# Optimization experiments

Measured on AMD Instinct MI355X. Metric: run time of the kernel, lower is better.

The kernel has to match this reference:

```python
import jax, jax.numpy as jnp
import numpy as np

ENC, PRED, H, V, DMAX = 1024, 640, 640, 1024, 4
B, T, U = 4, 256, 64


def setup_inputs() -> dict:
    key = jax.random.key(0)
    ks = jax.random.split(key, 10)
    s = lambda d: 1.0 / np.sqrt(d)
    return {
        "encoder_out": jax.random.normal(ks[0], (B, T, ENC), jnp.float32),
        "predictor_out": jax.random.normal(ks[1], (B, U, PRED), jnp.float32),
        "W_enc": jax.random.uniform(ks[2], (H, ENC), jnp.float32, -s(ENC), s(ENC)),
        "b_enc": jax.random.uniform(ks[3], (H,), jnp.float32, -s(ENC), s(ENC)),
        "W_pred": jax.random.uniform(ks[4], (H, PRED), jnp.float32, -s(PRED), s(PRED)),
        "b_pred": jax.random.uniform(ks[5], (H,), jnp.float32, -s(PRED), s(PRED)),
        "W_out": jax.random.uniform(ks[6], (V, H), jnp.float32, -s(H), s(H)),
        "b_out": jax.random.uniform(ks[7], (V,), jnp.float32, -s(H), s(H)),
        "W_dur": jax.random.uniform(ks[8], (DMAX + 1, H), jnp.float32, -s(H), s(H)),
        "b_dur": jax.random.uniform(ks[9], (DMAX + 1,), jnp.float32, -s(H), s(H)),
    }


def reference(encoder_out, predictor_out, W_enc, b_enc, W_pred, b_pred,
              W_out, b_out, W_dur, b_dur):
    # Project encoder [B,T,H] and predictor [B,U,H]
    enc = jnp.einsum('bte,he->bth', encoder_out, W_enc) + b_enc
    pred = jnp.einsum('bup,hp->buh', predictor_out, W_pred) + b_pred
    # Broadcast-add -> [B,T,U,H], tanh
    joint = jnp.tanh(enc[:, :, None, :] + pred[:, None, :, :])
    # Dual heads
    logits = jnp.einsum('btuh,vh->btuv', joint, W_out) + b_out        # [B,T,U,V]
    durations = jnp.einsum('btuh,dh->btud', joint, W_dur) + b_dur     # [B,T,U,DMAX+1]
    return (logits, durations)
```

## Files before the change

kernel.cpp:

```cpp
#include <hip/hip_runtime.h>

typedef unsigned short u16;
typedef unsigned int u32;

typedef __bf16 bf16x8 __attribute__((ext_vector_type(8)));
typedef float f32x4 __attribute__((ext_vector_type(4)));

union FragI { int4 i; bf16x8 b; };
union FragU { bf16x8 b; u16 u[8]; };

__device__ __forceinline__ u16 f2bf(float x) {
  u32 u = __float_as_uint(x);
  u32 r = (u + 0x7fffu + ((u >> 16) & 1u)) >> 16;
  return (u16)r;
}

__device__ __forceinline__ float tanh_fast(float x) {
  float e = __expf(2.0f * x);
  return 1.0f - __fdividef(2.0f, e + 1.0f);
}

__device__ __forceinline__ bf16x8 load_cvt8(const float* __restrict__ p) {
  float4 f0 = *(const float4*)p;
  float4 f1 = *(const float4*)(p + 4);
  FragU t;
  t.u[0] = f2bf(f0.x); t.u[1] = f2bf(f0.y); t.u[2] = f2bf(f0.z); t.u[3] = f2bf(f0.w);
  t.u[4] = f2bf(f1.x); t.u[5] = f2bf(f1.y); t.u[6] = f2bf(f1.z); t.u[7] = f2bf(f1.w);
  return t.b;
}

#define GLDS(gptr, lptr) \
  __builtin_amdgcn_global_load_lds((const __attribute__((address_space(1))) u32*)(gptr), \
                                   (__attribute__((address_space(3))) u32*)(lptr), 16, 0, 0)

__global__ __launch_bounds__(256) void conv_v4(const float* __restrict__ in,
                                               u16* __restrict__ out, int n4) {
  int i = blockIdx.x * 256 + threadIdx.x;
  if (i >= n4) return;
  float4 f = ((const float4*)in)[i];
  union { u16 u[4]; int2 v; } o;
  o.u[0] = f2bf(f.x); o.u[1] = f2bf(f.y); o.u[2] = f2bf(f.z); o.u[3] = f2bf(f.w);
  ((int2*)out)[i] = o.v;
}

__global__ __launch_bounds__(256) void proj_gemm(const float* __restrict__ A,
                                                 const float* __restrict__ Bw,
                                                 const float* __restrict__ bias,
                                                 float* __restrict__ C,
                                                 int M, int N, int K) {
  int tid = threadIdx.x;
  int lane = tid & 63, wid = tid >> 6;
  int m0 = blockIdx.x * 64, n0 = blockIdx.y * 64;
  int kper = K >> 2;
  int kbase = wid * kper;
  int ksteps = kper >> 5;
  int r16 = lane & 15, khi = (lane >> 4) * 8;

  f32x4 z = {0.f, 0.f, 0.f, 0.f};
  f32x4 acc[4][4];
  for (int i = 0; i < 4; ++i)
    for (int j = 0; j < 4; ++j) acc[i][j] = z;

  for (int ks = 0; ks < ksteps; ++ks) {
    int k = kbase + ks * 32 + khi;
    bf16x8 af[4], bf[4];
#pragma unroll
    for (int fm = 0; fm < 4; ++fm)
      af[fm] = load_cvt8(A + (size_t)(m0 + fm * 16 + r16) * K + k);
#pragma unroll
    for (int fn = 0; fn < 4; ++fn)
      bf[fn] = load_cvt8(Bw + (size_t)(n0 + fn * 16 + r16) * K + k);
#pragma unroll
    for (int fm = 0; fm < 4; ++fm)
#pragma unroll
      for (int fn = 0; fn < 4; ++fn)
        acc[fm][fn] = __builtin_amdgcn_mfma_f32_16x16x32_bf16(af[fm], bf[fn], acc[fm][fn], 0, 0, 0);
  }

  __shared__ float red[4][64][64];
#pragma unroll
  for (int fm = 0; fm < 4; ++fm)
#pragma unroll
    for (int fn = 0; fn < 4; ++fn)
#pragma unroll
      for (int i = 0; i < 4; ++i)
        red[wid][fm * 16 + (lane >> 4) * 4 + i][fn * 16 + r16] = acc[fm][fn][i];
  __syncthreads();
  for (int idx = tid; idx < 4096; idx += 256) {
    int r = idx >> 6, c = idx & 63;
    float s = red[0][r][c] + red[1][r][c] + red[2][r][c] + red[3][r][c] + bias[n0 + c];
    C[(size_t)(m0 + r) * N + n0 + c] = s;
  }
}

__global__ __launch_bounds__(256) void joint_tanh(const float* __restrict__ enc,
                                                  const float* __restrict__ pred,
                                                  u16* __restrict__ J) {
  const int total = 65536 * 80;
  for (int c = blockIdx.x * 256 + threadIdx.x; c < total; c += gridDim.x * 256) {
    int m = c / 80;
    int j = c - m * 80;
    int bt = m >> 6;
    int uu = m & 63;
    int b = bt >> 8;
    const float* ep = enc + bt * 640 + j * 8;
    const float* pp = pred + (b * 64 + uu) * 640 + j * 8;
    float4 e0 = *(const float4*)ep;
    float4 e1 = *(const float4*)(ep + 4);
    float4 p0 = *(const float4*)pp;
    float4 p1 = *(const float4*)(pp + 4);
    union { u16 u[8]; int4 v; } o;
    o.u[0] = f2bf(tanh_fast(e0.x + p0.x));
    o.u[1] = f2bf(tanh_fast(e0.y + p0.y));
    o.u[2] = f2bf(tanh_fast(e0.z + p0.z));
    o.u[3] = f2bf(tanh_fast(e0.w + p0.w));
    o.u[4] = f2bf(tanh_fast(e1.x + p1.x));
    o.u[5] = f2bf(tanh_fast(e1.y + p1.y));
    o.u[6] = f2bf(tanh_fast(e1.z + p1.z));
    o.u[7] = f2bf(tanh_fast(e1.w + p1.w));
    *(int4*)(J + (size_t)c * 8) = o.v;
  }
}

#define LOGITS_N 67108864
#define WS_LD 648

__device__ __forceinline__ void stage_half(const u16* __restrict__ g, u16* l,
                                           int wid, int lane) {
  int rl = wid * 8 + (lane >> 3);
  int cl = ((lane & 7) ^ (lane >> 3)) * 8;
  const u16* gp = g + (size_t)rl * 640 + cl;
  u16* lp = l + wid * 512;
  GLDS(gp, lp);
  GLDS(gp + (size_t)64 * 640, lp + 4096);
}

__global__ __launch_bounds__(512, 2) void main_gemm(const u16* __restrict__ J,
                                                    const u16* __restrict__ Wo,
                                                    const float* __restrict__ W_dur,
                                                    const float* __restrict__ b_out,
                                                    const float* __restrict__ b_dur,
                                                    float* __restrict__ out) {
  __shared__ __align__(16) u16 As[2][16384];
  __shared__ __align__(16) u16 Bs[2][16384];
  __shared__ __align__(16) u16 Ws[16 * WS_LD];

  int tid = threadIdx.x;
  int lane = tid & 63, wid = tid >> 6;
  int bid = blockIdx.x;
  int swz = (bid & 7) * 128 + (bid >> 3);
  int bn = swz & 3, bm = swz >> 2;
  int m0 = bm * 256, n0 = bn * 256;
  int wr = wid >> 2, wc = wid & 3;
  int r16 = lane & 15, khi8 = (lane >> 4) * 8;
  int xorv = (r16 & 7) << 3;
  bool dur_blk = (bn == 0);
  bool do_dur = dur_blk && (wc == 0);

  if (dur_blk) {
    for (int i = tid; i < 16 * WS_LD; i += 512) {
      int r = i / WS_LD, c = i - r * WS_LD;
      Ws[i] = (r < 5 && c < 640) ? f2bf(W_dur[r * 640 + c]) : (u16)0;
    }
  }
  const u16* JA = J + (size_t)m0 * 640;
  const u16* WB = Wo + (size_t)n0 * 640;
  stage_half(JA, As[0], wid, lane);
  stage_half(JA + (size_t)128 * 640, As[0] + 8192, wid, lane);
  stage_half(WB, Bs[0], wid, lane);
  stage_half(WB + (size_t)128 * 640, Bs[0] + 8192, wid, lane);
  asm volatile("s_waitcnt lgkmcnt(0)" ::: "memory");
  __builtin_amdgcn_sched_barrier(0);

  f32x4 z = {0.f, 0.f, 0.f, 0.f};
  f32x4 acc[8][4];
#pragma unroll
  for (int i = 0; i < 8; ++i)
#pragma unroll
    for (int j = 0; j < 4; ++j) acc[i][j] = z;
  f32x4 dacc[8];
#pragma unroll
  for (int i = 0; i < 8; ++i) dacc[i] = z;

  FragI bfr[4][2], wd[2];

  for (int it = 0; it < 5; ++it) {
    int t0 = 2 * it;
#pragma unroll
    for (int p = 0; p < 8; ++p) {
      const int q = p & 3;
      const int b = p >> 2;
      const int tc = t0 + b;

      if (q == 0) {
        asm volatile("s_waitcnt vmcnt(0)" ::: "memory");
        __builtin_amdgcn_sched_barrier(0);
        __builtin_amdgcn_s_barrier();
        __builtin_amdgcn_sched_barrier(0);
      }

      const u16* Ab = As[b];
      const u16* Bb = Bs[b];
      FragI aq[2][2];
#pragma unroll
      for (int m = 0; m < 2; ++m)
#pragma unroll
        for (int ks = 0; ks < 2; ++ks)
          aq[m][ks].i = *(const int4*)(Ab + (wr * 128 + q * 32 + m * 16 + r16) * 64 +
                                       ((ks * 32 + khi8) ^ xorv));
      if (q == 0) {
#pragma unroll
        for (int fn = 0; fn < 4; ++fn)
#pragma unroll
          for (int ks = 0; ks < 2; ++ks)
            bfr[fn][ks].i = *(const int4*)(Bb + (wc * 64 + fn * 16 + r16) * 64 +
                                           ((ks * 32 + khi8) ^ xorv));
        if (do_dur) {
#pragma unroll
          for (int ks = 0; ks < 2; ++ks)
            wd[ks].i = *(const int4*)(Ws + r16 * WS_LD + tc * 64 + ks * 32 + khi8);
        }
      }

      if (b == 0 || it < 4) {
        const int ts = t0 + 1 + b;
        u16* dA = As[1 - b];
        u16* dB = Bs[1 - b];
        if (p == 0 || p == 4) stage_half(JA + (size_t)ts * 64, dA, wid, lane);
        if (p == 1 || p == 5) stage_half(JA + (size_t)(128 * 640) + ts * 64, dA + 8192, wid, lane);
        if (p == 2 || p == 6) stage_half(WB + (size_t)ts * 64, dB, wid, lane);
        if (p == 3 || p == 7) stage_half(WB + (size_t)(128 * 640) + ts * 64, dB + 8192, wid, lane);
      }

      if (q != 0) {
        __builtin_amdgcn_s_barrier();
      }
      asm volatile("s_waitcnt lgkmcnt(0)" ::: "memory");
      __builtin_amdgcn_sched_barrier(0);

      __builtin_amdgcn_s_setprio(1);
#pragma unroll
      for (int m = 0; m < 2; ++m) {
#pragma unroll
        for (int ks = 0; ks < 2; ++ks) {
#pragma unroll
          for (int fn = 0; fn < 4; ++fn)
            acc[q * 2 + m][fn] = __builtin_amdgcn_mfma_f32_16x16x32_bf16(
                aq[m][ks].b, bfr[fn][ks].b, acc[q * 2 + m][fn], 0, 0, 0);
          if (do_dur)
            dacc[q * 2 + m] = __builtin_amdgcn_mfma_f32_16x16x32_bf16(
                aq[m][ks].b, wd[ks].b, dacc[q * 2 + m], 0, 0, 0);
        }
      }
      __builtin_amdgcn_s_setprio(0);
      __builtin_amdgcn_sched_barrier(0);
      __builtin_amdgcn_s_barrier();
    }
  }

  int rb = m0 + wr * 128 + (lane >> 4) * 4;
  int cb = n0 + wc * 64 + r16;
#pragma unroll
  for (int fn = 0; fn < 4; ++fn) {
    int col = cb + fn * 16;
    float bo = b_out[col];
#pragma unroll
    for (int fm = 0; fm < 8; ++fm) {
      int row = rb + fm * 16;
#pragma unroll
      for (int i = 0; i < 4; ++i)
        out[(size_t)(row + i) * 1024 + col] = acc[fm][fn][i] + bo;
    }
  }
  if (do_dur && r16 < 5) {
    float bd = b_dur[r16];
#pragma unroll
    for (int fm = 0; fm < 8; ++fm) {
      int row = rb + fm * 16;
#pragma unroll
      for (int i = 0; i < 4; ++i)
        out[LOGITS_N + (size_t)(row + i) * 5 + r16] = dacc[fm][i] + bd;
    }
  }
}

extern "C" void kernel_launch(void* const* d_in, const int* in_sizes, int n_in,
                              void* d_out, int out_size, void* d_ws, size_t ws_size,
                              hipStream_t stream) {
  const float* encoder   = (const float*)d_in[0];
  const float* predictor = (const float*)d_in[1];
  const float* W_enc = (const float*)d_in[2];
  const float* b_enc = (const float*)d_in[3];
  const float* W_pred = (const float*)d_in[4];
  const float* b_pred = (const float*)d_in[5];
  const float* W_out = (const float*)d_in[6];
  const float* b_out = (const float*)d_in[7];
  const float* W_dur = (const float*)d_in[8];
  const float* b_dur = (const float*)d_in[9];
  float* out = (float*)d_out;

  char* ws = (char*)d_ws;
  u16* Jbuf    = (u16*)(ws);
  u16* WoutB   = (u16*)(ws + 83886080);
  float* encP  = (float*)(ws + 85196800);
  float* predP = (float*)(ws + 87818240);

  conv_v4<<<640, 256, 0, stream>>>(W_out, WoutB, 163840);
  proj_gemm<<<dim3(16, 10), 256, 0, stream>>>(encoder, W_enc, b_enc, encP, 1024, 640, 1024);
  proj_gemm<<<dim3(4, 10), 256, 0, stream>>>(predictor, W_pred, b_pred, predP, 256, 640, 640);
  joint_tanh<<<2048, 256, 0, stream>>>(encP, predP, Jbuf);
  main_gemm<<<1024, 512, 0, stream>>>(Jbuf, WoutB, W_dur, b_out, b_dur, out);
}
```

Baseline: 209.7 us.

## Fuse joint tanh into main GEMM A-tile staging, drop materialized joint buffer

Removes the separate joint_tanh kernel and its 80MB bf16 joint buffer. The main GEMM now builds each A tile in registers from bf16 encoder and predictor projections, applying tanh before writing to LDS. The K loop is restructured into a simpler double-buffered loop with one barrier per K step. Projections are stored as bf16, which adds a rounding step before tanh, and each block recomputes tanh for its tile (four times across N blocks), putting transcendental work inside the GEMM pipeline.

```diff
diff --git a/kernel.cpp b/kernel.cpp
--- a/kernel.cpp
+++ b/kernel.cpp
@@ -6,24 +6,24 @@
 typedef __bf16 bf16x8 __attribute__((ext_vector_type(8)));
 typedef float f32x4 __attribute__((ext_vector_type(4)));
 
-union FragI { int4 i; bf16x8 b; };
-union FragU { bf16x8 b; u16 u[8]; };
+union FragI { int4 i; bf16x8 b; u16 u[8]; };
 
 __device__ __forceinline__ u16 f2bf(float x) {
   u32 u = __float_as_uint(x);
   u32 r = (u + 0x7fffu + ((u >> 16) & 1u)) >> 16;
   return (u16)r;
 }
-
+__device__ __forceinline__ float bf2f(u16 h) {
+  return __uint_as_float((u32)h << 16);
+}
 __device__ __forceinline__ float tanh_fast(float x) {
   float e = __expf(2.0f * x);
   return 1.0f - __fdividef(2.0f, e + 1.0f);
 }
-
 __device__ __forceinline__ bf16x8 load_cvt8(const float* __restrict__ p) {
   float4 f0 = *(const float4*)p;
   float4 f1 = *(const float4*)(p + 4);
-  FragU t;
+  union { bf16x8 b; u16 u[8]; } t;
   t.u[0] = f2bf(f0.x); t.u[1] = f2bf(f0.y); t.u[2] = f2bf(f0.z); t.u[3] = f2bf(f0.w);
   t.u[4] = f2bf(f1.x); t.u[5] = f2bf(f1.y); t.u[6] = f2bf(f1.z); t.u[7] = f2bf(f1.w);
   return t.b;
@@ -43,11 +43,11 @@
   ((int2*)out)[i] = o.v;
 }
 
-__global__ __launch_bounds__(256) void proj_gemm(const float* __restrict__ A,
-                                                 const float* __restrict__ Bw,
-                                                 const float* __restrict__ bias,
-                                                 float* __restrict__ C,
-                                                 int M, int N, int K) {
+__global__ __launch_bounds__(256) void proj_gemm_bf(const float* __restrict__ A,
+                                                    const float* __restrict__ Bw,
+                                                    const float* __restrict__ bias,
+                                                    u16* __restrict__ C,
+                                                    int M, int N, int K) {
   int tid = threadIdx.x;
   int lane = tid & 63, wid = tid >> 6;
   int m0 = blockIdx.x * 64, n0 = blockIdx.y * 64;
@@ -89,58 +89,31 @@
   for (int idx = tid; idx < 4096; idx += 256) {
     int r = idx >> 6, c = idx & 63;
     float s = red[0][r][c] + red[1][r][c] + red[2][r][c] + red[3][r][c] + bias[n0 + c];
-    C[(size_t)(m0 + r) * N + n0 + c] = s;
-  }
-}
-
-__global__ __launch_bounds__(256) void joint_tanh(const float* __restrict__ enc,
-                                                  const float* __restrict__ pred,
-                                                  u16* __restrict__ J) {
-  const int total = 65536 * 80;
-  for (int c = blockIdx.x * 256 + threadIdx.x; c < total; c += gridDim.x * 256) {
-    int m = c / 80;
-    int j = c - m * 80;
-    int bt = m >> 6;
-    int uu = m & 63;
-    int b = bt >> 8;
-    const float* ep = enc + bt * 640 + j * 8;
-    const float* pp = pred + (b * 64 + uu) * 640 + j * 8;
-    float4 e0 = *(const float4*)ep;
-    float4 e1 = *(const float4*)(ep + 4);
-    float4 p0 = *(const float4*)pp;
-    float4 p1 = *(const float4*)(pp + 4);
-    union { u16 u[8]; int4 v; } o;
-    o.u[0] = f2bf(tanh_fast(e0.x + p0.x));
-    o.u[1] = f2bf(tanh_fast(e0.y + p0.y));
-    o.u[2] = f2bf(tanh_fast(e0.z + p0.z));
-    o.u[3] = f2bf(tanh_fast(e0.w + p0.w));
-    o.u[4] = f2bf(tanh_fast(e1.x + p1.x));
-    o.u[5] = f2bf(tanh_fast(e1.y + p1.y));
-    o.u[6] = f2bf(tanh_fast(e1.z + p1.z));
-    o.u[7] = f2bf(tanh_fast(e1.w + p1.w));
-    *(int4*)(J + (size_t)c * 8) = o.v;
+    C[(size_t)(m0 + r) * N + n0 + c] = f2bf(s);
   }
 }
 
 #define LOGITS_N 67108864
 #define WS_LD 648
 
-__device__ __forceinline__ void stage_half(const u16* __restrict__ g, u16* l,
-                                           int wid, int lane) {
+__device__ __forceinline__ void stage_b(const u16* __restrict__ g, u16* l,
+                                        int wid, int lane) {
   int rl = wid * 8 + (lane >> 3);
   int cl = ((lane & 7) ^ (lane >> 3)) * 8;
   const u16* gp = g + (size_t)rl * 640 + cl;
   u16* lp = l + wid * 512;
-  GLDS(gp, lp);
-  GLDS(gp + (size_t)64 * 640, lp + 4096);
-}
-
-__global__ __launch_bounds__(512, 2) void main_gemm(const u16* __restrict__ J,
-                                                    const u16* __restrict__ Wo,
-                                                    const float* __restrict__ W_dur,
-                                                    const float* __restrict__ b_out,
-                                                    const float* __restrict__ b_dur,
-                                                    float* __restrict__ out) {
+#pragma unroll
+  for (int j = 0; j < 4; ++j)
+    GLDS(gp + (size_t)j * 64 * 640, lp + j * 4096);
+}
+
+__global__ __launch_bounds__(512, 2) void main_fused(const u16* __restrict__ encB,
+                                                     const u16* __restrict__ predB,
+                                                     const u16* __restrict__ WoB,
+                                                     const float* __restrict__ W_dur,
+                                                     const float* __restrict__ b_out,
+                                                     const float* __restrict__ b_dur,
+                                                     float* __restrict__ out) {
   __shared__ __align__(16) u16 As[2][16384];
   __shared__ __align__(16) u16 Bs[2][16384];
   __shared__ __align__(16) u16 Ws[16 * WS_LD];
@@ -157,20 +130,37 @@
   bool dur_blk = (bn == 0);
   bool do_dur = dur_blk && (wc == 0);
 
+  int ur = tid >> 3, kc = tid & 7;
+  int bt0 = bm * 4;
+  int pb = (bt0 >> 8) * 64;
+  const u16* prp = predB + (size_t)(pb + ur) * 640 + kc * 8;
+  const u16* enp = encB + (size_t)bt0 * 640 + kc * 8;
+  int aw_off = ur * 64 + ((kc ^ (ur & 7)) << 3);
+
   if (dur_blk) {
     for (int i = tid; i < 16 * WS_LD; i += 512) {
       int r = i / WS_LD, c = i - r * WS_LD;
       Ws[i] = (r < 5 && c < 640) ? f2bf(W_dur[r * 640 + c]) : (u16)0;
     }
   }
-  const u16* JA = J + (size_t)m0 * 640;
-  const u16* WB = Wo + (size_t)n0 * 640;
-  stage_half(JA, As[0], wid, lane);
-  stage_half(JA + (size_t)128 * 640, As[0] + 8192, wid, lane);
-  stage_half(WB, Bs[0], wid, lane);
-  stage_half(WB + (size_t)128 * 640, Bs[0] + 8192, wid, lane);
+
+  const u16* WB = WoB + (size_t)n0 * 640;
+
+  stage_b(WB, Bs[0], wid, lane);
+  {
+    int4 pr = *(const int4*)(prp);
+#pragma unroll
+    for (int j = 0; j < 4; ++j) {
+      int4 ev = *(const int4*)(enp + (size_t)j * 640);
+      FragI e, q, h;
+      e.i = ev; q.i = pr;
+#pragma unroll
+      for (int x = 0; x < 8; ++x)
+        h.u[x] = f2bf(tanh_fast(bf2f(e.u[x]) + bf2f(q.u[x])));
+      *(int4*)(As[0] + j * 4096 + aw_off) = h.i;
+    }
+  }
   asm volatile("s_waitcnt lgkmcnt(0)" ::: "memory");
-  __builtin_amdgcn_sched_barrier(0);
 
   f32x4 z = {0.f, 0.f, 0.f, 0.f};
   f32x4 acc[8][4];
@@ -182,25 +172,38 @@
 #pragma unroll
   for (int i = 0; i < 8; ++i) dacc[i] = z;
 
-  FragI bfr[4][2], wd[2];
-
-  for (int it = 0; it < 5; ++it) {
-    int t0 = 2 * it;
-#pragma unroll
-    for (int p = 0; p < 8; ++p) {
-      const int q = p & 3;
-      const int b = p >> 2;
-      const int tc = t0 + b;
-
-      if (q == 0) {
-        asm volatile("s_waitcnt vmcnt(0)" ::: "memory");
-        __builtin_amdgcn_sched_barrier(0);
-        __builtin_amdgcn_s_barrier();
-        __builtin_amdgcn_sched_barrier(0);
-      }
-
-      const u16* Ab = As[b];
-      const u16* Bb = Bs[b];
+#pragma unroll 2
+  for (int t = 0; t < 10; ++t) {
+    const int p = t & 1;
+    __builtin_amdgcn_s_barrier();
+    __builtin_amdgcn_sched_barrier(0);
+
+    int4 pr; int4 er[4];
+    if (t < 9) {
+      stage_b(WB + (t + 1) * 64, Bs[1 - p], wid, lane);
+      pr = *(const int4*)(prp + (t + 1) * 64);
+#pragma unroll
+      for (int j = 0; j < 4; ++j)
+        er[j] = *(const int4*)(enp + (size_t)j * 640 + (t + 1) * 64);
+    }
+    __builtin_amdgcn_sched_barrier(0);
+
+    const u16* Ab = As[p];
+    const u16* Bb = Bs[p];
+    FragI bfr[4][2], wd[2];
+#pragma unroll
+    for (int fn = 0; fn < 4; ++fn)
+#pragma unroll
+      for (int ks = 0; ks < 2; ++ks)
+        bfr[fn][ks].i = *(const int4*)(Bb + (wc * 64 + fn * 16 + r16) * 64 +
+                                       ((ks * 32 + khi8) ^ xorv));
+    if (do_dur) {
+#pragma unroll
+      for (int ks = 0; ks < 2; ++ks)
+        wd[ks].i = *(const int4*)(Ws + r16 * WS_LD + t * 64 + ks * 32 + khi8);
+    }
+#pragma unroll
+    for (int q = 0; q < 4; ++q) {
       FragI aq[2][2];
 #pragma unroll
       for (int m = 0; m < 2; ++m)
@@ -208,39 +211,9 @@
         for (int ks = 0; ks < 2; ++ks)
           aq[m][ks].i = *(const int4*)(Ab + (wr * 128 + q * 32 + m * 16 + r16) * 64 +
                                        ((ks * 32 + khi8) ^ xorv));
-      if (q == 0) {
-#pragma unroll
-        for (int fn = 0; fn < 4; ++fn)
-#pragma unroll
-          for (int ks = 0; ks < 2; ++ks)
-            bfr[fn][ks].i = *(const int4*)(Bb + (wc * 64 + fn * 16 + r16) * 64 +
-                                           ((ks * 32 + khi8) ^ xorv));
-        if (do_dur) {
-#pragma unroll
-          for (int ks = 0; ks < 2; ++ks)
-            wd[ks].i = *(const int4*)(Ws + r16 * WS_LD + tc * 64 + ks * 32 + khi8);
-        }
-      }
-
-      if (b == 0 || it < 4) {
-        const int ts = t0 + 1 + b;
-        u16* dA = As[1 - b];
-        u16* dB = Bs[1 - b];
-        if (p == 0 || p == 4) stage_half(JA + (size_t)ts * 64, dA, wid, lane);
-        if (p == 1 || p == 5) stage_half(JA + (size_t)(128 * 640) + ts * 64, dA + 8192, wid, lane);
-        if (p == 2 || p == 6) stage_half(WB + (size_t)ts * 64, dB, wid, lane);
-        if (p == 3 || p == 7) stage_half(WB + (size_t)(128 * 640) + ts * 64, dB + 8192, wid, lane);
-      }
-
-      if (q != 0) {
-        __builtin_amdgcn_s_barrier();
-      }
-      asm volatile("s_waitcnt lgkmcnt(0)" ::: "memory");
-      __builtin_amdgcn_sched_barrier(0);
-
       __builtin_amdgcn_s_setprio(1);
 #pragma unroll
-      for (int m = 0; m < 2; ++m) {
+      for (int m = 0; m < 2; ++m)
 #pragma unroll
         for (int ks = 0; ks < 2; ++ks) {
 #pragma unroll
@@ -251,11 +224,24 @@
             dacc[q * 2 + m] = __builtin_amdgcn_mfma_f32_16x16x32_bf16(
                 aq[m][ks].b, wd[ks].b, dacc[q * 2 + m], 0, 0, 0);
         }
+      __builtin_amdgcn_s_setprio(0);
+    }
+    __builtin_amdgcn_sched_barrier(0);
+
+    if (t < 9) {
+      u16* Ad = As[1 - p];
+#pragma unroll
+      for (int j = 0; j < 4; ++j) {
+        FragI e, q2, h;
+        e.i = er[j]; q2.i = pr;
+#pragma unroll
+        for (int x = 0; x < 8; ++x)
+          h.u[x] = f2bf(tanh_fast(bf2f(e.u[x]) + bf2f(q2.u[x])));
+        *(int4*)(Ad + j * 4096 + aw_off) = h.i;
       }
-      __builtin_amdgcn_s_setprio(0);
-      __builtin_amdgcn_sched_barrier(0);
-      __builtin_amdgcn_s_barrier();
-    }
+    }
+    asm volatile("s_waitcnt lgkmcnt(0)" ::: "memory");
+    __builtin_amdgcn_sched_barrier(0);
   }
 
   int rb = m0 + wr * 128 + (lane >> 4) * 4;
@@ -300,14 +286,12 @@
   float* out = (float*)d_out;
 
   char* ws = (char*)d_ws;
-  u16* Jbuf    = (u16*)(ws);
-  u16* WoutB   = (u16*)(ws + 83886080);
-  float* encP  = (float*)(ws + 85196800);
-  float* predP = (float*)(ws + 87818240);
-
-  conv_v4<<<640, 256, 0, stream>>>(W_out, WoutB, 163840);
-  proj_gemm<<<dim3(16, 10), 256, 0, stream>>>(encoder, W_enc, b_enc, encP, 1024, 640, 1024);
-  proj_gemm<<<dim3(4, 10), 256, 0, stream>>>(predictor, W_pred, b_pred, predP, 256, 640, 640);
-  joint_tanh<<<2048, 256, 0, stream>>>(encP, predP, Jbuf);
-  main_gemm<<<1024, 512, 0, stream>>>(Jbuf, WoutB, W_dur, b_out, b_dur, out);
-}
+  u16* WoB   = (u16*)(ws);
+  u16* encB  = (u16*)(ws + 1310720);
+  u16* predB = (u16*)(ws + 2621440);
+
+  conv_v4<<<640, 256, 0, stream>>>(W_out, WoB, 163840);
+  proj_gemm_bf<<<dim3(16, 10), 256, 0, stream>>>(encoder, W_enc, b_enc, encB, 1024, 640, 1024);
+  proj_gemm_bf<<<dim3(4, 10), 256, 0, stream>>>(predictor, W_pred, b_pred, predB, 256, 640, 640);
+  main_fused<<<1024, 512, 0, stream>>>(encB, predB, WoB, W_dur, b_out, b_dur, out);
+}
```

New measurement: 295.0 us. 40.7% more time.
